# Performance work log

Measured on AMD Instinct MI355X. Metric: run time of the kernel, lower is better.

## Reference

```python
import jax, jax.numpy as jnp
import numpy as np

NEG = -1e9

def mask_from_lens(src_lens, lip_lens, Tx, Ty):
    # [B, Tx, Ty] valid mask
    mx = jnp.arange(Tx)[None, :] < src_lens[:, None]
    my = jnp.arange(Ty)[None, :] < lip_lens[:, None]
    return (mx[:, :, None] & my[:, None, :]).astype(jnp.float32)

def maximum_path(value, mask):
    # Monotonic alignment search (VITS-style). value, mask: [B, Tx, Ty]
    B, Tx, Ty = value.shape
    value = value * mask
    xr = jnp.arange(Tx)[None, :]

    def fwd(v, inp):
        val_j, j = inp
        v0 = jnp.concatenate([jnp.full((B, 1), NEG, value.dtype), v[:, :-1]], axis=1)
        stay = v >= v0                      # True: best prev is same x
        vmax = jnp.where(stay, v, v0)
        vnew = jnp.where(xr <= j, vmax + val_j, NEG)
        return vnew, stay

    val_T = jnp.transpose(value, (2, 0, 1))          # [Ty,B,Tx]
    _, dirs = jax.lax.scan(fwd, jnp.zeros((B, Tx), value.dtype),
                           (val_T, jnp.arange(Ty)))
    mask_T = jnp.transpose(mask, (2, 0, 1)) > 0
    dirs = jnp.where(mask_T, dirs, True)             # padded cols: stay

    idx0 = mask[:, :, 0].sum(1).astype(jnp.int32) - 1  # src_lens - 1
    br = jnp.arange(B)

    def bwd(index, dir_j):
        onehot = jax.nn.one_hot(index, Tx, dtype=value.dtype)
        d = dir_j[br, index]
        return index + d.astype(jnp.int32) - 1, onehot

    _, path = jax.lax.scan(bwd, idx0, dirs, reverse=True)  # [Ty,B,Tx]
    return jnp.transpose(path, (1, 2, 0)) * mask

def setup_inputs() -> dict:
    key = jax.random.key(0)
    k1, k2, k3, k4, k5 = jax.random.split(key, 5)
    B, Ts, Tl, D = 32, 512, 2048, 256
    lip_motion_embedding = jax.random.normal(k1, (B, Tl, D), jnp.float32)
    output_phoneme = jax.random.normal(k2, (B, Ts, D), jnp.float32)
    src_lens = jax.random.randint(k3, (B,), Ts // 2, Ts + 1, jnp.int32)
    lip_lens = jax.random.randint(k4, (B,), Tl // 2, Tl + 1, jnp.int32)
    d_targets = jax.random.randint(k5, (B, Ts), 1, 8, jnp.int32)
    d_targets = jnp.where(jnp.arange(Ts)[None, :] < src_lens[:, None], d_targets, 0)
    return {"lip_motion_embedding": lip_motion_embedding,
            "output_phoneme": output_phoneme,
            "d_targets": d_targets,
            "src_lens": src_lens,
            "lip_lens": lip_lens}

def reference(lip_motion_embedding, output_phoneme, d_targets, src_lens, lip_lens):
    B, Tl, D = lip_motion_embedding.shape
    Ts = output_phoneme.shape[1]

    # mean expansion coefficient
    mean_cof = (d_targets.sum(-1) / lip_lens).mean()

    # normalized similarity  [B, Ts, Tl]
    norm_lip = lip_motion_embedding / jnp.linalg.norm(lip_motion_embedding, axis=2, keepdims=True)
    text_norm_base = jnp.linalg.norm(output_phoneme, axis=2, keepdims=True)
    norm_text = jnp.nan_to_num(output_phoneme / (text_norm_base + 1), nan=1.0)
    similarity = jnp.einsum('bld,bsd->bsl', norm_lip, norm_text)

    # duration targets rescaled to lip frame rate
    cofs = d_targets.sum(1) / lip_lens                      # [B]
    lip_targets = jnp.round(d_targets / cofs[:, None])      # [B, Ts] float
    dif = lip_lens.astype(lip_targets.dtype) - lip_targets.sum(1)
    max_idx = jnp.argmax(lip_targets, axis=1)
    lip_targets = lip_targets.at[jnp.arange(B), max_idx].add(dif)

    # gt_similarity: contiguous segments of ones per phoneme (vectorized scatter)
    lt = lip_targets.astype(jnp.int32)
    ends = jnp.cumsum(lt, axis=1)                           # [B, Ts]
    begins = ends - lt
    kk = jnp.arange(Tl)[None, None, :]
    gt_similarity = ((kk >= begins[:, :, None]) & (kk < ends[:, :, None])).astype(similarity.dtype)

    mask_sim = mask_from_lens(src_lens, lip_lens, Ts, Tl)
    alignment = maximum_path(similarity, mask_sim)
    d_predictions = jax.lax.stop_gradient(alignment.sum(-1)) * mean_cof

    return similarity, gt_similarity, alignment, d_predictions
```

## Files before the change

kernel.cpp:

```cpp
#include <hip/hip_runtime.h>
#include <math.h>

#define BATCH 32
#define TS    512
#define TL    2048
#define DD    256
#define NEGV  -1e9f

#define SIM_OFF   ((size_t)0)
#define GT_OFF    ((size_t)BATCH*TS*TL)
#define ALIGN_OFF ((size_t)2*BATCH*TS*TL)
#define DPRED_OFF ((size_t)3*BATCH*TS*TL)

#define WS_MEAN   0
#define WS_COF    256
#define WS_LSCALE 512
#define WS_TSCALE 262656
#define WS_BEGIN  328192
#define WS_END    393728
#define WS_START2 459264
#define WS_END2   524800

__global__ __launch_bounds__(256) void norm_kernel(const float* __restrict__ lip,
                                                   const float* __restrict__ phon,
                                                   float* __restrict__ lip_scale,
                                                   float* __restrict__ text_scale) {
    const int wave = threadIdx.x >> 6, lane = threadIdx.x & 63;
    const int row = blockIdx.x * 4 + wave;
    const int NL = BATCH * TL;
    const float* src = (row < NL) ? (lip + (size_t)row * DD)
                                  : (phon + (size_t)(row - NL) * DD);
    float4 q = *(const float4*)(src + lane * 4);
    float ss = q.x*q.x + q.y*q.y + q.z*q.z + q.w*q.w;
    #pragma unroll
    for (int off = 32; off; off >>= 1) ss += __shfl_xor(ss, off);
    if (lane == 0) {
        if (row < NL) lip_scale[row] = 1.0f / sqrtf(ss);
        else          text_scale[row - NL] = 1.0f / (sqrtf(ss) + 1.0f);
    }
}

__global__ __launch_bounds__(512) void prep_kernel(const int* __restrict__ d_targets,
                                                   const int* __restrict__ lip_lens,
                                                   int* __restrict__ begins,
                                                   int* __restrict__ ends,
                                                   float* __restrict__ cof_arr) {
    __shared__ int   si[512];
    __shared__ float sf[512];
    __shared__ int   sx[512];
    const int b = blockIdx.x, t = threadIdx.x;
    const int d = d_targets[b * TS + t];
    const int lipL = lip_lens[b];

    si[t] = d; __syncthreads();
    for (int off = 256; off; off >>= 1) { if (t < off) si[t] += si[t + off]; __syncthreads(); }
    const int sum_d = si[0]; __syncthreads();

    const float cofv = (float)sum_d / (float)lipL;
    float lt = rintf((float)d / cofv);

    sf[t] = lt; __syncthreads();
    for (int off = 256; off; off >>= 1) { if (t < off) sf[t] += sf[t + off]; __syncthreads(); }
    const float sumlt = sf[0]; __syncthreads();
    const float dif = (float)lipL - sumlt;

    sf[t] = lt; sx[t] = t; __syncthreads();
    for (int off = 256; off; off >>= 1) {
        if (t < off) {
            float v2 = sf[t + off]; int i2 = sx[t + off];
            if (v2 > sf[t] || (v2 == sf[t] && i2 < sx[t])) { sf[t] = v2; sx[t] = i2; }
        }
        __syncthreads();
    }
    const int max_idx = sx[0]; __syncthreads();
    if (t == max_idx) lt += dif;
    const int li = (int)lt;

    si[t] = li; __syncthreads();
    for (int off = 1; off < 512; off <<= 1) {
        int add = (t >= off) ? si[t - off] : 0;
        __syncthreads();
        si[t] += add;
        __syncthreads();
    }
    const int e = si[t];
    begins[b * TS + t] = e - li;
    ends[b * TS + t]   = e;
    if (t == 0) cof_arr[b] = cofv;
}

#define G_STAGE(B, S)                                                          \
  { _Pragma("unroll")                                                          \
    for (int kk = 0; kk < 4; ++kk) {                                           \
      As[B][sub * 8 + kk][r]     = (&a0[S].x)[kk] * sA;                        \
      As[B][sub * 8 + 4 + kk][r] = (&a1[S].x)[kk] * sA;                        \
      Bs[B][sub * 8 + kk][r]     = (&b0[S].x)[kk] * sB;                        \
      Bs[B][sub * 8 + 4 + kk][r] = (&b1[S].x)[kk] * sB;                        \
    } }

#define G_COMPUTE(B)                                                           \
  { _Pragma("unroll")                                                          \
    for (int kk = 0; kk < 16; ++kk) {                                          \
      float4 t0 = *(const float4*)&As[B][kk][ty * 4];                          \
      float4 t1 = *(const float4*)&As[B][kk][64 + ty * 4];                     \
      float4 t2 = *(const float4*)&Bs[B][kk][tx * 4];                          \
      float4 t3 = *(const float4*)&Bs[B][kk][64 + tx * 4];                     \
      float a[8] = {t0.x, t0.y, t0.z, t0.w, t1.x, t1.y, t1.z, t1.w};           \
      float bbv[8] = {t2.x, t2.y, t2.z, t2.w, t3.x, t3.y, t3.z, t3.w};         \
      _Pragma("unroll")                                                        \
      for (int i = 0; i < 8; ++i)                                              \
        _Pragma("unroll")                                                      \
        for (int j = 0; j < 8; ++j)                                            \
          acc[i][j] = fmaf(a[i], bbv[j], acc[i][j]);                           \
    } }

#define G_ITER(KT, CB, NB)                                                     \
  {                                                                            \
    __syncthreads();                                                           \
    if ((KT) < 14) {                                                           \
      a0[CB] = *(const float4*)(Ag + ((KT) + 2) * 16);                         \
      a1[CB] = *(const float4*)(Ag + ((KT) + 2) * 16 + 4);                     \
      b0[CB] = *(const float4*)(Bg + ((KT) + 2) * 16);                         \
      b1[CB] = *(const float4*)(Bg + ((KT) + 2) * 16 + 4);                     \
    }                                                                          \
    if ((KT) < 15) G_STAGE(NB, NB);                                            \
    G_COMPUTE(CB);                                                             \
  }

__global__ __launch_bounds__(256) void gemm_kernel(const float* __restrict__ lip,
                                                   const float* __restrict__ phon,
                                                   const float* __restrict__ lip_scale,
                                                   const float* __restrict__ text_scale,
                                                   const int* __restrict__ begins,
                                                   const int* __restrict__ ends,
                                                   float* __restrict__ sim,
                                                   float* __restrict__ gt,
                                                   float* __restrict__ simT) {
    const int b = blockIdx.z, tm = blockIdx.y, tn = blockIdx.x;
    const int t = threadIdx.x;
    __shared__ __align__(16) float As[2][16][132];
    __shared__ __align__(16) float Bs[2][16][132];

    const int r = t >> 1, sub = t & 1;
    const int tx = t & 15, ty = t >> 4;

    const float* Ag = phon + ((size_t)(b * TS + tm * 128 + r)) * DD + sub * 8;
    const float* Bg = lip  + ((size_t)(b * TL + tn * 128 + r)) * DD + sub * 8;
    const float sA = text_scale[b * TS + tm * 128 + r];
    const float sB = lip_scale[b * TL + tn * 128 + r];

    float4 a0[2], a1[2], b0[2], b1[2];
    a0[0] = *(const float4*)(Ag);
    a1[0] = *(const float4*)(Ag + 4);
    b0[0] = *(const float4*)(Bg);
    b1[0] = *(const float4*)(Bg + 4);
    G_STAGE(0, 0);
    a0[1] = *(const float4*)(Ag + 16);
    a1[1] = *(const float4*)(Ag + 16 + 4);
    b0[1] = *(const float4*)(Bg + 16);
    b1[1] = *(const float4*)(Bg + 16 + 4);

    float acc[8][8];
    #pragma unroll
    for (int i = 0; i < 8; ++i)
        #pragma unroll
        for (int j = 0; j < 8; ++j) acc[i][j] = 0.0f;

    for (int kt = 0; kt < 16; kt += 2) {
        G_ITER(kt,     0, 1);
        G_ITER(kt + 1, 1, 0);
    }

    const size_t base = (size_t)b * TS * TL;
    #pragma unroll
    for (int mi = 0; mi < 2; ++mi) {
        #pragma unroll
        for (int im = 0; im < 4; ++im) {
            const int srow = tm * 128 + mi * 64 + ty * 4 + im;
            const int ai = mi * 4 + im;
            float* prow = sim + base + (size_t)srow * TL + tn * 128;
            float4 w0 = {acc[ai][0], acc[ai][1], acc[ai][2], acc[ai][3]};
            float4 w1 = {acc[ai][4], acc[ai][5], acc[ai][6], acc[ai][7]};
            *(float4*)(prow + tx * 4) = w0;
            *(float4*)(prow + 64 + tx * 4) = w1;

            const int bg = begins[b * TS + srow], en = ends[b * TS + srow];
            const int l0 = tn * 128 + tx * 4;
            float4 g0, g1;
            g0.x = (l0 + 0 >= bg && l0 + 0 < en) ? 1.f : 0.f;
            g0.y = (l0 + 1 >= bg && l0 + 1 < en) ? 1.f : 0.f;
            g0.z = (l0 + 2 >= bg && l0 + 2 < en) ? 1.f : 0.f;
            g0.w = (l0 + 3 >= bg && l0 + 3 < en) ? 1.f : 0.f;
            g1.x = (l0 + 64 >= bg && l0 + 64 < en) ? 1.f : 0.f;
            g1.y = (l0 + 65 >= bg && l0 + 65 < en) ? 1.f : 0.f;
            g1.z = (l0 + 66 >= bg && l0 + 66 < en) ? 1.f : 0.f;
            g1.w = (l0 + 67 >= bg && l0 + 67 < en) ? 1.f : 0.f;
            float* grow = gt + base + (size_t)srow * TL + tn * 128;
            *(float4*)(grow + tx * 4) = g0;
            *(float4*)(grow + 64 + tx * 4) = g1;
        }
    }

    {
        float* tb = simT + (size_t)b * TL * TS + (size_t)(tn * 128) * TS + tm * 128;
        #pragma unroll
        for (int bj = 0; bj < 8; ++bj) {
            const int lloc = (bj < 4) ? (tx * 4 + bj) : (64 + tx * 4 + (bj - 4));
            float* trow = tb + (size_t)lloc * TS;
            float4 w0 = {acc[0][bj], acc[1][bj], acc[2][bj], acc[3][bj]};
            float4 w1 = {acc[4][bj], acc[5][bj], acc[6][bj], acc[7][bj]};
            *(float4*)(trow + ty * 4) = w0;
            *(float4*)(trow + 64 + ty * 4) = w1;
        }
    }
}

#define DP_WAVES 4

template <bool CHK>
__device__ __forceinline__ void dp32(const float (&c0)[32], const float (&c1)[32],
                                     int j0, int x0, int lane,
                                     float xm0, float xm1,
                                     float& v0, float& v1,
                                     unsigned& w0, unsigned& w1,
                                     const float (&bw)[32], float (&bbf)[32]) {
    #pragma unroll
    for (int s = 0; s < 32; ++s) {
        const int j = j0 + s;
        float up = __shfl_up(v1, 1);
        up = (lane == 0) ? bw[s] : up;
        const float ov0 = v0;
        const unsigned st0 = (v0 >= up)  ? 1u : 0u;
        const unsigned st1 = (v1 >= ov0) ? 1u : 0u;
        float nv0 = fmaf(c0[s], xm0, fmaxf(v0, up));
        float nv1 = fmaf(c1[s], xm1, fmaxf(v1, ov0));
        if (CHK) {
            nv0 = (x0     <= j) ? nv0 : NEGV;
            nv1 = (x0 + 1 <= j) ? nv1 : NEGV;
        }
        w0 = w0 * 2u + st0;
        w1 = w1 * 2u + st1;
        bbf[s] = nv1;
        v0 = nv0; v1 = nv1;
    }
}

__device__ __forceinline__ void dp_superstep(const float* __restrict__ simTb,
                                             unsigned* __restrict__ dirs_lds,
                                             float* __restrict__ bndl,
                                             float (&cur0)[32], float (&cur1)[32],
                                             float (&nxt0)[32], float (&nxt1)[32],
                                             int T, int k, int lane, int x0, int nchunks,
                                             float xm0, float xm1,
                                             float& v0, float& v1,
                                             unsigned& w0, unsigned& w1) {
    __syncthreads();
    const int c  = T - k;
    const int cp = c + 1;
    if (cp >= 0 && cp < nchunks) {
        const int j0p = cp << 5;
        #pragma unroll
        for (int s = 0; s < 32; ++s) {
            float2 q = *(const float2*)(simTb + (size_t)(j0p + s) * TS + x0);
            nxt0[s] = q.x; nxt1[s] = q.y;
        }
    }
    if (c >= 0 && c < nchunks) {
        const int j0 = c << 5;
        float bw[32];
        if (k > 0) {
            const float* br = bndl + (k - 1) * 96;
            const int r0 = j0 % 96;
            { float4 bq = *(const float4*)(br + ((r0 + 92) % 96)); bw[0] = bq.w; }
            #pragma unroll
            for (int q = 0; q < 8; ++q) {
                float4 bq = *(const float4*)(br + r0 + (q << 2));
                bw[4 * q + 1] = bq.x;
                bw[4 * q + 2] = bq.y;
                bw[4 * q + 3] = bq.z;
                if (4 * q + 4 < 32) bw[4 * q + 4] = bq.w;
            }
        } else {
            #pragma unroll
            for (int s = 0; s < 32; ++s) bw[s] = NEGV;
        }
        float bbf[32];
        if (c < 16) dp32<true >(cur0, cur1, j0, x0, lane, xm0, xm1, v0, v1, w0, w1, bw, bbf);
        else        dp32<false>(cur0, cur1, j0, x0, lane, xm0, xm1, v0, v1, w0, w1, bw, bbf);
        if (lane == 63) {
            float* brw = bndl + k * 96 + (j0 % 96);
            #pragma unroll
            for (int q = 0; q < 8; ++q) {
                float4 w4 = {bbf[4*q], bbf[4*q+1], bbf[4*q+2], bbf[4*q+3]};
                *(float4*)(brw + 4 * q) = w4;
            }
        }
        dirs_lds[c * 512 + x0]     = w0;
        dirs_lds[c * 512 + x0 + 1] = w1;
        w0 = 0u; w1 = 0u;
    }
}

__global__ __launch_bounds__(256, 1) void dp_kernel(const float* __restrict__ simT,
                                                    const int* __restrict__ src_lens,
                                                    const int* __restrict__ lip_lens,
                                                    const float* __restrict__ cof_arr,
                                                    float* __restrict__ mean_out,
                                                    int* __restrict__ start2,
                                                    int* __restrict__ end2) {
    __shared__ unsigned dirs_lds[64 * 512];
    __shared__ __align__(16) float bndl[DP_WAVES * 96];

    const int b = blockIdx.x, tid = threadIdx.x;
    const int k = tid >> 6, lane = tid & 63;
    const int x0 = (k << 7) + (lane << 1);

    if (b == 0 && tid == 0) {
        float s = 0.f;
        for (int i = 0; i < BATCH; ++i) s += cof_arr[i];
        mean_out[0] = s / 32.0f;
    }
    for (int i = tid; i < DP_WAVES * 96; i += 256) bndl[i] = 0.f;

    const int srcL = src_lens[b], lipL = lip_lens[b];
    const float* simTb = simT + (size_t)b * TL * TS;
    const int nchunks = (lipL + 31) >> 5;

    const float xm0 = (x0     < srcL) ? 1.f : 0.f;
    const float xm1 = (x0 + 1 < srcL) ? 1.f : 0.f;
    float v0 = 0.f, v1 = 0.f;
    unsigned w0 = 0u, w1 = 0u;

    float curA0[32], curA1[32], curB0[32], curB1[32];
    if (k == 0) {
        #pragma unroll
        for (int s = 0; s < 32; ++s) {
            float2 q = *(const float2*)(simTb + (size_t)s * TS + x0);
            curA0[s] = q.x; curA1[s] = q.y;
        }
    }

    const int tot = nchunks + DP_WAVES - 1;
    for (int t = 0; t < tot; t += 2) {
        dp_superstep(simTb, dirs_lds, bndl, curA0, curA1, curB0, curB1,
                     t, k, lane, x0, nchunks, xm0, xm1, v0, v1, w0, w1);
        if (t + 1 < tot)
            dp_superstep(simTb, dirs_lds, bndl, curB0, curB1, curA0, curA1,
                         t + 1, k, lane, x0, nchunks, xm0, xm1, v0, v1, w0, w1);
    }

    start2[b * TS + tid]       = 0;
    end2[b * TS + tid]         = 0;
    start2[b * TS + tid + 256] = 0;
    end2[b * TS + tid + 256]   = 0;
    asm volatile("s_waitcnt vmcnt(0)" ::: "memory");
    __syncthreads();

    if (k == 0) {
        int x = srcL - 1;
        if (lane == 0) end2[b * TS + x] = lipL;
        int j = lipL - 1;
        while (x > 0 && j >= 0) {
            const unsigned W = dirs_lds[(j >> 5) * 512 + x];
            const int jj = j & 31;
            const unsigned m = (~W) & (0xFFFFFFFFu << (31 - jj));
            if (m == 0u) { j -= jj + 1; continue; }
            const int jp = __builtin_ctz(m);
            const int jprime = (j & ~31) + (31 - jp);
            if (lane == 0) { start2[b * TS + x] = jprime; end2[b * TS + x - 1] = jprime; }
            x -= 1; j = jprime - 1;
        }
    }
}

__global__ __launch_bounds__(256) void align_kernel(const int* __restrict__ start2,
                                                    const int* __restrict__ end2,
                                                    const float* __restrict__ mean_cof,
                                                    float* __restrict__ alignOut,
                                                    float* __restrict__ dpred) {
    const int s = blockIdx.x, b = blockIdx.y, t = threadIdx.x;
    const int st = start2[b * TS + s], en = end2[b * TS + s];
    float* row = alignOut + ((size_t)b * TS + s) * TL;
    const int l0 = t * 8;
    float4 r0, r1;
    r0.x = (l0 + 0 >= st && l0 + 0 < en) ? 1.f : 0.f;
    r0.y = (l0 + 1 >= st && l0 + 1 < en) ? 1.f : 0.f;
    r0.z = (l0 + 2 >= st && l0 + 2 < en) ? 1.f : 0.f;
    r0.w = (l0 + 3 >= st && l0 + 3 < en) ? 1.f : 0.f;
    r1.x = (l0 + 4 >= st && l0 + 4 < en) ? 1.f : 0.f;
    r1.y = (l0 + 5 >= st && l0 + 5 < en) ? 1.f : 0.f;
    r1.z = (l0 + 6 >= st && l0 + 6 < en) ? 1.f : 0.f;
    r1.w = (l0 + 7 >= st && l0 + 7 < en) ? 1.f : 0.f;
    *(float4*)(row + l0) = r0;
    *(float4*)(row + l0 + 4) = r1;
    if (t == 0) dpred[b * TS + s] = (float)(en - st) * mean_cof[0];
}

extern "C" void kernel_launch(void* const* d_in, const int* in_sizes, int n_in,
                              void* d_out, int out_size, void* d_ws, size_t ws_size,
                              hipStream_t stream) {
    const float* lip   = (const float*)d_in[0];
    const float* phon  = (const float*)d_in[1];
    const int* d_tg    = (const int*)d_in[2];
    const int* src_l   = (const int*)d_in[3];
    const int* lip_l   = (const int*)d_in[4];
    float* out = (float*)d_out;

    char* ws = (char*)d_ws;
    float*    mean_cof   = (float*)(ws + WS_MEAN);
    float*    cof_arr    = (float*)(ws + WS_COF);
    float*    lip_scale  = (float*)(ws + WS_LSCALE);
    float*    text_scale = (float*)(ws + WS_TSCALE);
    int*      begins     = (int*)(ws + WS_BEGIN);
    int*      ends       = (int*)(ws + WS_END);
    int*      start2     = (int*)(ws + WS_START2);
    int*      end2       = (int*)(ws + WS_END2);

    float* sim   = out + SIM_OFF;
    float* gt    = out + GT_OFF;
    float* aln   = out + ALIGN_OFF;
    float* dpred = out + DPRED_OFF;

    norm_kernel<<<(BATCH * TL + BATCH * TS) / 4, 256, 0, stream>>>(lip, phon, lip_scale, text_scale);
    prep_kernel<<<BATCH, 512, 0, stream>>>(d_tg, lip_l, begins, ends, cof_arr);
    gemm_kernel<<<dim3(TL / 128, TS / 128, BATCH), 256, 0, stream>>>(lip, phon, lip_scale, text_scale,
                                                                     begins, ends, sim, gt, aln);
    dp_kernel<<<BATCH, 256, 0, stream>>>(aln, src_l, lip_l, cof_arr, mean_cof, start2, end2);
    align_kernel<<<dim3(TS, BATCH), 256, 0, stream>>>(start2, end2, mean_cof, aln, dpred);
}
```

Measured before the change: 1.042 ms.

## Deepen DP chunk prefetch to two ahead and single-buffer GEMM LDS tiles

The DP wavefront kernel now prefetches the similarity chunk two steps ahead using a three-buffer register rotation selected by a phase counter, instead of one step ahead with two buffers. This is meant to hide more global-load latency behind the serial DP recurrence. The GEMM kernel drops its double-buffered LDS staging in favour of a single buffer with two barriers per k-step and a register prefetch of the next slice. That halves LDS use, which may raise occupancy, but adds a barrier per step. The extra 64 register floats per lane and the runtime phase branching in the DP kernel risk spills or register pressure.

```diff
diff --git a/kernel.cpp b/kernel.cpp
--- a/kernel.cpp
+++ b/kernel.cpp
@@ -89,44 +89,6 @@
     if (t == 0) cof_arr[b] = cofv;
 }
 
-#define G_STAGE(B, S)                                                          \
-  { _Pragma("unroll")                                                          \
-    for (int kk = 0; kk < 4; ++kk) {                                           \
-      As[B][sub * 8 + kk][r]     = (&a0[S].x)[kk] * sA;                        \
-      As[B][sub * 8 + 4 + kk][r] = (&a1[S].x)[kk] * sA;                        \
-      Bs[B][sub * 8 + kk][r]     = (&b0[S].x)[kk] * sB;                        \
-      Bs[B][sub * 8 + 4 + kk][r] = (&b1[S].x)[kk] * sB;                        \
-    } }
-
-#define G_COMPUTE(B)                                                           \
-  { _Pragma("unroll")                                                          \
-    for (int kk = 0; kk < 16; ++kk) {                                          \
-      float4 t0 = *(const float4*)&As[B][kk][ty * 4];                          \
-      float4 t1 = *(const float4*)&As[B][kk][64 + ty * 4];                     \
-      float4 t2 = *(const float4*)&Bs[B][kk][tx * 4];                          \
-      float4 t3 = *(const float4*)&Bs[B][kk][64 + tx * 4];                     \
-      float a[8] = {t0.x, t0.y, t0.z, t0.w, t1.x, t1.y, t1.z, t1.w};           \
-      float bbv[8] = {t2.x, t2.y, t2.z, t2.w, t3.x, t3.y, t3.z, t3.w};         \
-      _Pragma("unroll")                                                        \
-      for (int i = 0; i < 8; ++i)                                              \
-        _Pragma("unroll")                                                      \
-        for (int j = 0; j < 8; ++j)                                            \
-          acc[i][j] = fmaf(a[i], bbv[j], acc[i][j]);                           \
-    } }
-
-#define G_ITER(KT, CB, NB)                                                     \
-  {                                                                            \
-    __syncthreads();                                                           \
-    if ((KT) < 14) {                                                           \
-      a0[CB] = *(const float4*)(Ag + ((KT) + 2) * 16);                         \
-      a1[CB] = *(const float4*)(Ag + ((KT) + 2) * 16 + 4);                     \
-      b0[CB] = *(const float4*)(Bg + ((KT) + 2) * 16);                         \
-      b1[CB] = *(const float4*)(Bg + ((KT) + 2) * 16 + 4);                     \
-    }                                                                          \
-    if ((KT) < 15) G_STAGE(NB, NB);                                            \
-    G_COMPUTE(CB);                                                             \
-  }
-
 __global__ __launch_bounds__(256) void gemm_kernel(const float* __restrict__ lip,
                                                    const float* __restrict__ phon,
                                                    const float* __restrict__ lip_scale,
@@ -138,8 +100,8 @@
                                                    float* __restrict__ simT) {
     const int b = blockIdx.z, tm = blockIdx.y, tn = blockIdx.x;
     const int t = threadIdx.x;
-    __shared__ __align__(16) float As[2][16][132];
-    __shared__ __align__(16) float Bs[2][16][132];
+    __shared__ __align__(16) float As[16][132];
+    __shared__ __align__(16) float Bs[16][132];
 
     const int r = t >> 1, sub = t & 1;
     const int tx = t & 15, ty = t >> 4;
@@ -149,16 +111,10 @@
     const float sA = text_scale[b * TS + tm * 128 + r];
     const float sB = lip_scale[b * TL + tn * 128 + r];
 
-    float4 a0[2], a1[2], b0[2], b1[2];
-    a0[0] = *(const float4*)(Ag);
-    a1[0] = *(const float4*)(Ag + 4);
-    b0[0] = *(const float4*)(Bg);
-    b1[0] = *(const float4*)(Bg + 4);
-    G_STAGE(0, 0);
-    a0[1] = *(const float4*)(Ag + 16);
-    a1[1] = *(const float4*)(Ag + 16 + 4);
-    b0[1] = *(const float4*)(Bg + 16);
-    b1[1] = *(const float4*)(Bg + 16 + 4);
+    float4 ra0 = *(const float4*)(Ag);
+    float4 ra1 = *(const float4*)(Ag + 4);
+    float4 rb0 = *(const float4*)(Bg);
+    float4 rb1 = *(const float4*)(Bg + 4);
 
     float acc[8][8];
     #pragma unroll
@@ -166,9 +122,40 @@
         #pragma unroll
         for (int j = 0; j < 8; ++j) acc[i][j] = 0.0f;
 
-    for (int kt = 0; kt < 16; kt += 2) {
-        G_ITER(kt,     0, 1);
-        G_ITER(kt + 1, 1, 0);
+    for (int kt = 0; kt < 16; ++kt) {
+        __syncthreads();
+        {
+            const float* pa0 = &ra0.x; const float* pa1 = &ra1.x;
+            const float* pb0 = &rb0.x; const float* pb1 = &rb1.x;
+            #pragma unroll
+            for (int kk = 0; kk < 4; ++kk) {
+                As[sub * 8 + kk][r]     = pa0[kk] * sA;
+                As[sub * 8 + 4 + kk][r] = pa1[kk] * sA;
+                Bs[sub * 8 + kk][r]     = pb0[kk] * sB;
+                Bs[sub * 8 + 4 + kk][r] = pb1[kk] * sB;
+            }
+        }
+        __syncthreads();
+        if (kt < 15) {
+            ra0 = *(const float4*)(Ag + (kt + 1) * 16);
+            ra1 = *(const float4*)(Ag + (kt + 1) * 16 + 4);
+            rb0 = *(const float4*)(Bg + (kt + 1) * 16);
+            rb1 = *(const float4*)(Bg + (kt + 1) * 16 + 4);
+        }
+        #pragma unroll
+        for (int kk = 0; kk < 16; ++kk) {
+            float4 t0 = *(const float4*)&As[kk][ty * 4];
+            float4 t1 = *(const float4*)&As[kk][64 + ty * 4];
+            float4 t2 = *(const float4*)&Bs[kk][tx * 4];
+            float4 t3 = *(const float4*)&Bs[kk][64 + tx * 4];
+            float a[8] = {t0.x, t0.y, t0.z, t0.w, t1.x, t1.y, t1.z, t1.w};
+            float bb[8] = {t2.x, t2.y, t2.z, t2.w, t3.x, t3.y, t3.z, t3.w};
+            #pragma unroll
+            for (int i = 0; i < 8; ++i)
+                #pragma unroll
+                for (int j = 0; j < 8; ++j)
+                    acc[i][j] = fmaf(a[i], bb[j], acc[i][j]);
+        }
     }
 
     const size_t base = (size_t)b * TS * TL;
@@ -245,26 +232,30 @@
     }
 }
 
+__device__ __forceinline__ void dp_chunk_load(const float* __restrict__ simTb,
+                                              float (&d0)[32], float (&d1)[32],
+                                              int c, int x0) {
+    const int j0p = c << 5;
+    #pragma unroll
+    for (int s = 0; s < 32; ++s) {
+        float2 q = *(const float2*)(simTb + (size_t)(j0p + s) * TS + x0);
+        d0[s] = q.x; d1[s] = q.y;
+    }
+}
+
 __device__ __forceinline__ void dp_superstep(const float* __restrict__ simTb,
                                              unsigned* __restrict__ dirs_lds,
                                              float* __restrict__ bndl,
                                              float (&cur0)[32], float (&cur1)[32],
-                                             float (&nxt0)[32], float (&nxt1)[32],
+                                             float (&tgt0)[32], float (&tgt1)[32],
                                              int T, int k, int lane, int x0, int nchunks,
                                              float xm0, float xm1,
                                              float& v0, float& v1,
                                              unsigned& w0, unsigned& w1) {
-    __syncthreads();
-    const int c  = T - k;
-    const int cp = c + 1;
-    if (cp >= 0 && cp < nchunks) {
-        const int j0p = cp << 5;
-        #pragma unroll
-        for (int s = 0; s < 32; ++s) {
-            float2 q = *(const float2*)(simTb + (size_t)(j0p + s) * TS + x0);
-            nxt0[s] = q.x; nxt1[s] = q.y;
-        }
-    }
+    const int c   = T - k;
+    const int cp2 = c + 2;
+    if (cp2 >= 0 && cp2 < nchunks)
+        dp_chunk_load(simTb, tgt0, tgt1, cp2, x0);
     if (c >= 0 && c < nchunks) {
         const int j0 = c << 5;
         float bw[32];
@@ -331,22 +322,29 @@
     float v0 = 0.f, v1 = 0.f;
     unsigned w0 = 0u, w1 = 0u;
 
-    float curA0[32], curA1[32], curB0[32], curB1[32];
+    float cA0[32], cA1[32], cB0[32], cB1[32], cC0[32], cC1[32];
+
     if (k == 0) {
-        #pragma unroll
-        for (int s = 0; s < 32; ++s) {
-            float2 q = *(const float2*)(simTb + (size_t)s * TS + x0);
-            curA0[s] = q.x; curA1[s] = q.y;
-        }
+        dp_chunk_load(simTb, cA0, cA1, 0, x0);
+        dp_chunk_load(simTb, cB0, cB1, 1, x0);
+    } else if (k == 1) {
+        dp_chunk_load(simTb, cA0, cA1, 0, x0);
     }
 
     const int tot = nchunks + DP_WAVES - 1;
-    for (int t = 0; t < tot; t += 2) {
-        dp_superstep(simTb, dirs_lds, bndl, curA0, curA1, curB0, curB1,
-                     t, k, lane, x0, nchunks, xm0, xm1, v0, v1, w0, w1);
-        if (t + 1 < tot)
-            dp_superstep(simTb, dirs_lds, bndl, curB0, curB1, curA0, curA1,
-                         t + 1, k, lane, x0, nchunks, xm0, xm1, v0, v1, w0, w1);
+    int phase = (3 - (k % 3)) % 3;
+    for (int T = 0; T < tot; ++T) {
+        __syncthreads();
+        if (phase == 0)
+            dp_superstep(simTb, dirs_lds, bndl, cA0, cA1, cC0, cC1,
+                         T, k, lane, x0, nchunks, xm0, xm1, v0, v1, w0, w1);
+        else if (phase == 1)
+            dp_superstep(simTb, dirs_lds, bndl, cB0, cB1, cA0, cA1,
+                         T, k, lane, x0, nchunks, xm0, xm1, v0, v1, w0, w1);
+        else
+            dp_superstep(simTb, dirs_lds, bndl, cC0, cC1, cB0, cB1,
+                         T, k, lane, x0, nchunks, xm0, xm1, v0, v1, w0, w1);
+        phase = (phase + 1 == 3) ? 0 : phase + 1;
     }
 
     start2[b * TS + tid]       = 0;
```

Result: faster. 985.3 us (-5.5%).
